# Kernel tuning notes

Hardware: AMD Instinct MI355X
Metric: run time of the kernel (lower is better)

Reference implementation:

```python
import jax, jax.numpy as jnp
import numpy as np

B, N, M, D = 4, 2048, 4096, 1
C, K = 4, 32
POINTS_PER_UNIT = 20


def setup_inputs() -> dict:
    key = jax.random.key(0)
    k1, k2, k3 = jax.random.split(key, 3)
    xz = jax.random.uniform(k1, (M, D), dtype=jnp.float32) * 4.0 - 2.0  # grid locations
    x = jax.random.uniform(k2, (B, N, D), dtype=jnp.float32) * 4.0 - 2.0  # target locations
    z = jax.random.normal(k3, (B, C, M, K), dtype=jnp.float32)
    log_scale = jnp.array([np.log(2.0 / POINTS_PER_UNIT)], dtype=jnp.float32)
    return {"xz": xz, "x": x, "z": z, "log_scale": log_scale}


def reference(xz, x, z, log_scale):
    # pairwise squared distances between grid xz [M,D] and targets x [B,N,D] -> [B,M,N]
    d2 = jnp.sum((xz[None, :, None, :] - x[:, None, :, :]) ** 2, axis=-1)
    # RBF weights (note: divided by exp(log_scale), matching original code)
    w = jnp.exp(-0.5 * d2 / jnp.exp(log_scale[0]))  # [B,M,N]
    # weights^T @ z with channel broadcast: [B,C,N,K]
    zt = jnp.einsum('bmn,bcmk->bcnk', w, z)
    # outer product z @ z^T: [B,C,N,N] positive semi-definite
    out = jnp.einsum('bcnk,bcmk->bcnm', zt, zt)
    return (xz, out)
```

## Files before the change

### kernel.cpp

```cpp
#include <hip/hip_runtime.h>
#include <hip/hip_bf16.h>

#define B_  4
#define N_  2048
#define M_  4096
#define C_  4
#define K_  32
#define CK_ 128

typedef float f32x4 __attribute__((ext_vector_type(4)));
typedef short s16x8 __attribute__((ext_vector_type(8)));

__device__ __forceinline__ short f2bf(float f) {
    union { __hip_bfloat16 h; short s; } u;
    u.h = __float2bfloat16(f);
    return u.s;
}
__device__ __forceinline__ float bf2f(unsigned short u) {
    return __uint_as_float((unsigned)u << 16);
}

#define MT1 128
#define ZS  136

template <int MS>
__global__ __launch_bounds__(256, 4) void zt_mfma_kernel(
    const float* __restrict__ xz, const float* __restrict__ x,
    const float* __restrict__ z,  const float* __restrict__ ls,
    unsigned short* __restrict__ ztp)
{
    constexpr int MCH = M_ / MS;
    __shared__ __align__(16) float xz_s[MCH];
    __shared__ __align__(16) short z_s[CK_][ZS];

    const int tid  = threadIdx.x;
    const int lane = tid & 63;
    const int wave = tid >> 6;
    const int wn   = wave >> 1;
    const int wc   = wave & 1;
    const int ms   = blockIdx.x;
    const int nblk = blockIdx.y * 128;
    const int b    = blockIdx.z;
    const int l15  = lane & 15;
    const int lg   = lane >> 4;

    const float coef = -0.5f * __expf(-ls[0]);

    float xv[4];
    #pragma unroll
    for (int fa = 0; fa < 4; ++fa)
        xv[fa] = x[b * N_ + nblk + wn * 64 + fa * 16 + l15];

    const int mstart = ms * MCH;
    for (int i = tid; i < MCH; i += 256) xz_s[i] = xz[mstart + i];

    f32x4 acc[4][4];
    #pragma unroll
    for (int i = 0; i < 4; ++i)
        #pragma unroll
        for (int j = 0; j < 4; ++j) acc[i][j] = (f32x4)0.0f;

    for (int mc = 0; mc < MCH; mc += MT1) {
        __syncthreads();
        #pragma unroll
        for (int it = 0; it < CK_ * (MT1 / 4) / 256; ++it) {
            const int u  = tid + it * 256;
            const int ck = u & 127;
            const int mq = u >> 7;
            const int m  = mstart + mc + mq * 4;
            const float* zp = &z[(((size_t)b * C_ + (ck >> 5)) * M_ + m) * K_ + (ck & 31)];
            short4 pk;
            pk.x = f2bf(zp[0]);
            pk.y = f2bf(zp[K_]);
            pk.z = f2bf(zp[2 * K_]);
            pk.w = f2bf(zp[3 * K_]);
            *reinterpret_cast<short4*>(&z_s[ck][mq * 4]) = pk;
        }
        __syncthreads();
        #pragma unroll
        for (int ks = 0; ks < MT1 / 32; ++ks) {
            const float* xzp = &xz_s[mc + ks * 32 + lg * 8];
            const f32x4 t0 = *reinterpret_cast<const f32x4*>(xzp);
            const f32x4 t1 = *reinterpret_cast<const f32x4*>(xzp + 4);
            const float t[8] = {t0.x, t0.y, t0.z, t0.w, t1.x, t1.y, t1.z, t1.w};
            s16x8 af[4];
            #pragma unroll
            for (int fa = 0; fa < 4; ++fa) {
                #pragma unroll
                for (int j = 0; j < 8; ++j) {
                    const float d = t[j] - xv[fa];
                    af[fa][j] = f2bf(__expf(coef * d * d));
                }
            }
            s16x8 bfg[4];
            #pragma unroll
            for (int fc = 0; fc < 4; ++fc)
                bfg[fc] = *reinterpret_cast<const s16x8*>(
                    &z_s[wc * 64 + fc * 16 + l15][ks * 32 + lg * 8]);
            #pragma unroll
            for (int fa = 0; fa < 4; ++fa)
                #pragma unroll
                for (int fc = 0; fc < 4; ++fc)
                    acc[fa][fc] = __builtin_amdgcn_mfma_f32_16x16x32_bf16(
                        af[fa], bfg[fc], acc[fa][fc], 0, 0, 0);
        }
    }

    unsigned short* dst = ztp + (size_t)ms * (B_ * C_ * N_ * K_);
    #pragma unroll
    for (int fc = 0; fc < 4; ++fc) {
        const int ck = wc * 64 + fc * 16 + l15;
        const int c  = ck >> 5, k = ck & 31;
        #pragma unroll
        for (int fa = 0; fa < 4; ++fa) {
            const int n0 = nblk + wn * 64 + fa * 16 + lg * 4;
            #pragma unroll
            for (int r = 0; r < 4; ++r)
                dst[(((size_t)b * C_ + c) * N_ + n0 + r) * K_ + k] =
                    (unsigned short)f2bf(acc[fa][fc][r]);
        }
    }
}

template <int MS>
__global__ __launch_bounds__(256) void zt_reduce_copy_kernel(
    const unsigned short* __restrict__ ztp, unsigned short* __restrict__ ztb,
    const float* __restrict__ xz, float* __restrict__ out)
{
    if (blockIdx.x >= 1024) {
        const int t = (blockIdx.x - 1024) * 256 + threadIdx.x;
        *(float4*)&out[t * 4] = *(const float4*)&xz[t * 4];
        return;
    }
    const size_t t      = (size_t)blockIdx.x * 256 + threadIdx.x;
    const size_t stride = (size_t)(B_ * C_ * N_ * K_);
    float s0 = 0.f, s1 = 0.f, s2 = 0.f, s3 = 0.f;
    #pragma unroll
    for (int p = 0; p < MS; ++p) {
        const ushort4 v = *(const ushort4*)&ztp[(size_t)p * stride + t * 4];
        s0 += bf2f(v.x); s1 += bf2f(v.y); s2 += bf2f(v.z); s3 += bf2f(v.w);
    }
    ushort4 pk;
    pk.x = (unsigned short)f2bf(s0); pk.y = (unsigned short)f2bf(s1);
    pk.z = (unsigned short)f2bf(s2); pk.w = (unsigned short)f2bf(s3);
    *(ushort4*)&ztb[t * 4] = pk;
}

#define TB 128
__global__ __launch_bounds__(256, 4) void out_mfma_kernel(
    const unsigned short* __restrict__ ztb, float* __restrict__ out)
{
    __shared__ __align__(16) float t_s[64][132];

    const int tid  = threadIdx.x;
    const int lane = tid & 63;
    const int wave = tid >> 6;
    const int wn   = wave >> 1;
    const int wm   = wave & 1;
    const int l15  = lane & 15;
    const int lg   = lane >> 4;
    const int mblk = blockIdx.x * TB;
    const int nblk = blockIdx.y * TB;
    const int bc   = blockIdx.z;

    const unsigned short* base = ztb + (size_t)bc * (N_ * K_);

    s16x8 afr[4], bfr[4];
    #pragma unroll
    for (int f = 0; f < 4; ++f) {
        const int n = nblk + wn * 64 + f * 16 + l15;
        afr[f] = *reinterpret_cast<const s16x8*>(&base[(size_t)n * K_ + lg * 8]);
        const int m = mblk + wm * 64 + f * 16 + l15;
        bfr[f] = *reinterpret_cast<const s16x8*>(&base[(size_t)m * K_ + lg * 8]);
    }

    f32x4 acc[4][4];
    #pragma unroll
    for (int i = 0; i < 4; ++i)
        #pragma unroll
        for (int j = 0; j < 4; ++j) acc[i][j] = (f32x4)0.0f;

    #pragma unroll
    for (int fa = 0; fa < 4; ++fa)
        #pragma unroll
        for (int fm = 0; fm < 4; ++fm)
            acc[fa][fm] = __builtin_amdgcn_mfma_f32_16x16x32_bf16(
                afr[fa], bfr[fm], acc[fa][fm], 0, 0, 0);

    float* ob = out + (size_t)bc * N_ * N_;

    #pragma unroll
    for (int p = 0; p < 2; ++p) {
        if (p) __syncthreads();
        if (wn == p) {
            #pragma unroll
            for (int fa = 0; fa < 4; ++fa) {
                const int row0 = fa * 16 + lg * 4;
                #pragma unroll
                for (int fm = 0; fm < 4; ++fm) {
                    const int mcol = wm * 64 + fm * 16 + l15;
                    #pragma unroll
                    for (int r = 0; r < 4; ++r)
                        t_s[row0 + r][mcol] = acc[fa][fm][r];
                }
            }
        }
        __syncthreads();
        #pragma unroll
        for (int it = 0; it < 8; ++it) {
            const int e   = tid + it * 256;
            const int row = e >> 5;
            const int c4  = e & 31;
            const f32x4 v = *reinterpret_cast<const f32x4*>(&t_s[row][c4 * 4]);
            __builtin_nontemporal_store(
                v, (f32x4*)&ob[(size_t)(nblk + p * 64 + row) * N_ + mblk + c4 * 4]);
        }
    }
}

extern "C" void kernel_launch(void* const* d_in, const int* in_sizes, int n_in,
                              void* d_out, int out_size, void* d_ws, size_t ws_size,
                              hipStream_t stream)
{
    const float* xz = (const float*)d_in[0];
    const float* x  = (const float*)d_in[1];
    const float* z  = (const float*)d_in[2];
    const float* ls = (const float*)d_in[3];
    float* out = (float*)d_out;

    (void)in_sizes; (void)n_in; (void)out_size;

    const size_t ztf = (size_t)B_ * C_ * N_ * K_;
    unsigned short* ztb = (unsigned short*)d_ws;
    unsigned short* ztp = ztb + ztf;

    const size_t need16 = ztf * 2 + (size_t)16 * ztf * 2;
    const size_t need8  = ztf * 2 + (size_t)8  * ztf * 2;
    if (ws_size >= need16) {
        zt_mfma_kernel<16><<<dim3(16, N_ / 128, B_), dim3(256), 0, stream>>>(xz, x, z, ls, ztp);
        zt_reduce_copy_kernel<16><<<dim3(1028), dim3(256), 0, stream>>>(ztp, ztb, xz, out);
    } else if (ws_size >= need8) {
        zt_mfma_kernel<8><<<dim3(8, N_ / 128, B_), dim3(256), 0, stream>>>(xz, x, z, ls, ztp);
        zt_reduce_copy_kernel<8><<<dim3(1028), dim3(256), 0, stream>>>(ztp, ztb, xz, out);
    } else {
        zt_mfma_kernel<4><<<dim3(4, N_ / 128, B_), dim3(256), 0, stream>>>(xz, x, z, ls, ztp);
        zt_reduce_copy_kernel<4><<<dim3(1028), dim3(256), 0, stream>>>(ztp, ztb, xz, out);
    }

    out_mfma_kernel<<<dim3(N_ / TB, N_ / TB, B_ * C_), dim3(256), 0, stream>>>(ztb, out + M_);
}
```

Baseline: 85.55 us.

## Pre-transpose z to bf16 and double-buffer z tiles in 512-thread zt kernel

Adds a pre-pass kernel that converts z to bf16 in a transposed [b,ck,m] layout, so the main kernel can load z tiles with wide vector loads instead of strided scalar fp32 loads with per-element conversion. The zt kernel now uses 512 threads with each wave owning half the rows, and double-buffers shared-memory z tiles so the next tile's global loads overlap the current MFMA work. The M-split drops from 16 to 8, which lowers partial-sum traffic and reduce cost but leaves fewer blocks in flight. The extra pre-pass launch and the workspace needed for the transposed copy are the cost.

```diff
diff --git a/kernel.cpp b/kernel.cpp
--- a/kernel.cpp
+++ b/kernel.cpp
@@ -20,75 +20,106 @@
     return __uint_as_float((unsigned)u << 16);
 }
 
-#define MT1 128
-#define ZS  136
+__global__ __launch_bounds__(256) void z2bft_kernel(
+    const float* __restrict__ z, unsigned short* __restrict__ zbt)
+{
+    __shared__ float t_f[K_][136];
+    const int tid = threadIdx.x;
+    const int m0  = blockIdx.x * 128;
+    const int bc  = blockIdx.y;
+
+    #pragma unroll
+    for (int it = 0; it < 4; ++it) {
+        const int e = tid + it * 256;
+        const int m = e >> 3, k4 = e & 7;
+        const f32x4 v = *(const f32x4*)&z[((size_t)bc * M_ + m0 + m) * K_ + k4 * 4];
+        #pragma unroll
+        for (int j = 0; j < 4; ++j) t_f[k4 * 4 + j][m] = v[j];
+    }
+    __syncthreads();
+    #pragma unroll
+    for (int it = 0; it < 2; ++it) {
+        const int e = tid + it * 256;
+        const int r = e >> 4, mq = e & 15;
+        s16x8 pk;
+        #pragma unroll
+        for (int j = 0; j < 8; ++j) pk[j] = f2bf(t_f[r][mq * 8 + j]);
+        *(s16x8*)&zbt[((size_t)(bc * K_ + r)) * M_ + m0 + mq * 8] = pk;
+    }
+}
+
+#define ZS 136
 
 template <int MS>
-__global__ __launch_bounds__(256, 4) void zt_mfma_kernel(
+__global__ __launch_bounds__(512, 4) void zt_mfma_kernel(
     const float* __restrict__ xz, const float* __restrict__ x,
-    const float* __restrict__ z,  const float* __restrict__ ls,
+    const unsigned short* __restrict__ zbt, const float* __restrict__ ls,
     unsigned short* __restrict__ ztp)
 {
     constexpr int MCH = M_ / MS;
+    constexpr int NCH = MCH / 128;
     __shared__ __align__(16) float xz_s[MCH];
-    __shared__ __align__(16) short z_s[CK_][ZS];
+    __shared__ __align__(16) short z_s[2][CK_][ZS];
 
     const int tid  = threadIdx.x;
     const int lane = tid & 63;
-    const int wave = tid >> 6;
-    const int wn   = wave >> 1;
-    const int wc   = wave & 1;
+    const int w    = tid >> 6;
+    const int wq   = w >> 1;
+    const int wc   = w & 1;
+    const int l15  = lane & 15;
+    const int lg   = lane >> 4;
     const int ms   = blockIdx.x;
     const int nblk = blockIdx.y * 128;
     const int b    = blockIdx.z;
-    const int l15  = lane & 15;
-    const int lg   = lane >> 4;
 
     const float coef = -0.5f * __expf(-ls[0]);
 
-    float xv[4];
-    #pragma unroll
-    for (int fa = 0; fa < 4; ++fa)
-        xv[fa] = x[b * N_ + nblk + wn * 64 + fa * 16 + l15];
+    float xv[2];
+    #pragma unroll
+    for (int fa = 0; fa < 2; ++fa)
+        xv[fa] = x[b * N_ + nblk + wq * 32 + fa * 16 + l15];
 
     const int mstart = ms * MCH;
-    for (int i = tid; i < MCH; i += 256) xz_s[i] = xz[mstart + i];
-
-    f32x4 acc[4][4];
-    #pragma unroll
-    for (int i = 0; i < 4; ++i)
+    for (int i = tid; i < MCH; i += 512) xz_s[i] = xz[mstart + i];
+
+    f32x4 acc[2][4];
+    #pragma unroll
+    for (int i = 0; i < 2; ++i)
         #pragma unroll
         for (int j = 0; j < 4; ++j) acc[i][j] = (f32x4)0.0f;
 
-    for (int mc = 0; mc < MCH; mc += MT1) {
-        __syncthreads();
-        #pragma unroll
-        for (int it = 0; it < CK_ * (MT1 / 4) / 256; ++it) {
-            const int u  = tid + it * 256;
-            const int ck = u & 127;
-            const int mq = u >> 7;
-            const int m  = mstart + mc + mq * 4;
-            const float* zp = &z[(((size_t)b * C_ + (ck >> 5)) * M_ + m) * K_ + (ck & 31)];
-            short4 pk;
-            pk.x = f2bf(zp[0]);
-            pk.y = f2bf(zp[K_]);
-            pk.z = f2bf(zp[2 * K_]);
-            pk.w = f2bf(zp[3 * K_]);
-            *reinterpret_cast<short4*>(&z_s[ck][mq * 4]) = pk;
-        }
-        __syncthreads();
-        #pragma unroll
-        for (int ks = 0; ks < MT1 / 32; ++ks) {
-            const float* xzp = &xz_s[mc + ks * 32 + lg * 8];
+    s16x8 stg[4];
+    #define LOADC(t) { _Pragma("unroll")                                          \
+        for (int it = 0; it < 4; ++it) {                                          \
+            const int u = tid + it * 512;                                         \
+            const int ck = u >> 4, mq = u & 15;                                   \
+            stg[it] = *(const s16x8*)&zbt[((size_t)(b * CK_ + ck)) * M_ +         \
+                                          mstart + (t) * 128 + mq * 8];           \
+        } }
+    #define WRITEC(t) { _Pragma("unroll")                                         \
+        for (int it = 0; it < 4; ++it) {                                          \
+            const int u = tid + it * 512;                                         \
+            const int ck = u >> 4, mq = u & 15;                                   \
+            *(s16x8*)&z_s[(t) & 1][ck][mq * 8] = stg[it];                         \
+        } }
+
+    LOADC(0); WRITEC(0);
+    __syncthreads();
+
+    for (int t = 0; t < NCH; ++t) {
+        if (t + 1 < NCH) LOADC(t + 1);
+        #pragma unroll
+        for (int ks = 0; ks < 4; ++ks) {
+            const float* xzp = &xz_s[t * 128 + ks * 32 + lg * 8];
             const f32x4 t0 = *reinterpret_cast<const f32x4*>(xzp);
             const f32x4 t1 = *reinterpret_cast<const f32x4*>(xzp + 4);
-            const float t[8] = {t0.x, t0.y, t0.z, t0.w, t1.x, t1.y, t1.z, t1.w};
-            s16x8 af[4];
-            #pragma unroll
-            for (int fa = 0; fa < 4; ++fa) {
+            const float tt[8] = {t0.x, t0.y, t0.z, t0.w, t1.x, t1.y, t1.z, t1.w};
+            s16x8 af[2];
+            #pragma unroll
+            for (int fa = 0; fa < 2; ++fa) {
                 #pragma unroll
                 for (int j = 0; j < 8; ++j) {
-                    const float d = t[j] - xv[fa];
+                    const float d = tt[j] - xv[fa];
                     af[fa][j] = f2bf(__expf(coef * d * d));
                 }
             }
@@ -96,14 +127,16 @@
             #pragma unroll
             for (int fc = 0; fc < 4; ++fc)
                 bfg[fc] = *reinterpret_cast<const s16x8*>(
-                    &z_s[wc * 64 + fc * 16 + l15][ks * 32 + lg * 8]);
-            #pragma unroll
-            for (int fa = 0; fa < 4; ++fa)
+                    &z_s[t & 1][wc * 64 + fc * 16 + l15][ks * 32 + lg * 8]);
+            #pragma unroll
+            for (int fa = 0; fa < 2; ++fa)
                 #pragma unroll
                 for (int fc = 0; fc < 4; ++fc)
                     acc[fa][fc] = __builtin_amdgcn_mfma_f32_16x16x32_bf16(
                         af[fa], bfg[fc], acc[fa][fc], 0, 0, 0);
         }
+        if (t + 1 < NCH) WRITEC(t + 1);
+        __syncthreads();
     }
 
     unsigned short* dst = ztp + (size_t)ms * (B_ * C_ * N_ * K_);
@@ -112,14 +145,16 @@
         const int ck = wc * 64 + fc * 16 + l15;
         const int c  = ck >> 5, k = ck & 31;
         #pragma unroll
-        for (int fa = 0; fa < 4; ++fa) {
-            const int n0 = nblk + wn * 64 + fa * 16 + lg * 4;
+        for (int fa = 0; fa < 2; ++fa) {
+            const int n0 = nblk + wq * 32 + fa * 16 + lg * 4;
             #pragma unroll
             for (int r = 0; r < 4; ++r)
                 dst[(((size_t)b * C_ + c) * N_ + n0 + r) * K_ + k] =
                     (unsigned short)f2bf(acc[fa][fc][r]);
         }
     }
+    #undef LOADC
+    #undef WRITEC
 }
 
 template <int MS>
@@ -232,19 +267,21 @@
 
     const size_t ztf = (size_t)B_ * C_ * N_ * K_;
     unsigned short* ztb = (unsigned short*)d_ws;
-    unsigned short* ztp = ztb + ztf;
-
-    const size_t need16 = ztf * 2 + (size_t)16 * ztf * 2;
-    const size_t need8  = ztf * 2 + (size_t)8  * ztf * 2;
-    if (ws_size >= need16) {
-        zt_mfma_kernel<16><<<dim3(16, N_ / 128, B_), dim3(256), 0, stream>>>(xz, x, z, ls, ztp);
-        zt_reduce_copy_kernel<16><<<dim3(1028), dim3(256), 0, stream>>>(ztp, ztb, xz, out);
-    } else if (ws_size >= need8) {
-        zt_mfma_kernel<8><<<dim3(8, N_ / 128, B_), dim3(256), 0, stream>>>(xz, x, z, ls, ztp);
+    unsigned short* zbt = ztb + ztf;
+    unsigned short* ztp = zbt + (size_t)B_ * CK_ * M_;
+
+    z2bft_kernel<<<dim3(M_ / 128, B_ * C_), dim3(256), 0, stream>>>(z, zbt);
+
+    const size_t base_b = ztf * 2 + (size_t)B_ * CK_ * M_ * 2;
+    if (ws_size >= base_b + (size_t)8 * ztf * 2) {
+        zt_mfma_kernel<8><<<dim3(8, N_ / 128, B_), dim3(512), 0, stream>>>(xz, x, zbt, ls, ztp);
         zt_reduce_copy_kernel<8><<<dim3(1028), dim3(256), 0, stream>>>(ztp, ztb, xz, out);
+    } else if (ws_size >= base_b + (size_t)4 * ztf * 2) {
+        zt_mfma_kernel<4><<<dim3(4, N_ / 128, B_), dim3(512), 0, stream>>>(xz, x, zbt, ls, ztp);
+        zt_reduce_copy_kernel<4><<<dim3(1028), dim3(256), 0, stream>>>(ztp, ztb, xz, out);
     } else {
-        zt_mfma_kernel<4><<<dim3(4, N_ / 128, B_), dim3(256), 0, stream>>>(xz, x, z, ls, ztp);
-        zt_reduce_copy_kernel<4><<<dim3(1028), dim3(256), 0, stream>>>(ztp, ztb, xz, out);
+        zt_mfma_kernel<2><<<dim3(2, N_ / 128, B_), dim3(512), 0, stream>>>(xz, x, zbt, ls, ztp);
+        zt_reduce_copy_kernel<2><<<dim3(1028), dim3(256), 0, stream>>>(ztp, ztb, xz, out);
     }
 
     out_mfma_kernel<<<dim3(N_ / TB, N_ / TB, B_ * C_), dim3(256), 0, stream>>>(ztb, out + M_);
```

Result: faster. 82.16 us (-4.0%).
